# Performance work log

Measured on AMD Instinct MI355X. Metric: run time of the kernel, lower is better.

The kernel has to match this reference:

```python
import jax, jax.numpy as jnp
import numpy as np

B, S, E, H = 32, 2048, 512, 512


def setup_inputs() -> dict:
    key = jax.random.key(0)
    ks = jax.random.split(key, 6)
    scale = 1.0 / np.sqrt(H)  # PyTorch LSTM init range
    x = jax.random.normal(ks[0], (B, S, E), dtype=jnp.float32)
    lengths = jax.random.randint(ks[1], (B,), 1, S + 1, dtype=jnp.int32)
    W_ih = jax.random.uniform(ks[2], (4 * H, E), jnp.float32, -scale, scale)
    W_hh = jax.random.uniform(ks[3], (4 * H, H), jnp.float32, -scale, scale)
    b_ih = jax.random.uniform(ks[4], (4 * H,), jnp.float32, -scale, scale)
    b_hh = jax.random.uniform(ks[5], (4 * H,), jnp.float32, -scale, scale)
    return {"x": x, "lengths": lengths, "W_ih": W_ih, "W_hh": W_hh,
            "b_ih": b_ih, "b_hh": b_hh}


def _lstm_scan(x, W_ih, W_hh, b_ih, b_hh):
    # x: [B, S, E]. Precompute input projections for all timesteps (one big GEMM).
    x_proj = jnp.einsum('bse,ge->bsg', x, W_ih) + (b_ih + b_hh)  # [B, S, 4H]
    x_proj_t = jnp.swapaxes(x_proj, 0, 1)  # [S, B, 4H]

    def step(carry, xp_t):
        h, c = carry
        gates = xp_t + h @ W_hh.T  # [B, 4H]
        i, f, g, o = jnp.split(gates, 4, axis=-1)  # PyTorch gate order i,f,g,o
        i = jax.nn.sigmoid(i)
        f = jax.nn.sigmoid(f)
        g = jnp.tanh(g)
        o = jax.nn.sigmoid(o)
        c = f * c + i * g
        h = o * jnp.tanh(c)
        return (h, c), h

    h0 = jnp.zeros((B, H), dtype=x.dtype)
    c0 = jnp.zeros((B, H), dtype=x.dtype)
    (_, _), hs = jax.lax.scan(step, (h0, c0), x_proj_t)  # hs: [S, B, H]
    return hs


def reference(x, lengths, W_ih, W_hh, b_ih, b_hh):
    hs = _lstm_scan(x, W_ih, W_hh, b_ih, b_hh)  # [S, B, H]
    # zero-mask outputs at positions >= length (matches __maskLSTMOutput)
    mask = (jnp.arange(S)[:, None] < lengths[None, :]).astype(hs.dtype)  # [S, B]
    out = (hs * mask[:, :, None]).transpose(1, 0, 2)[:, :, None, :]  # [B, S, 1, H]
    # hidden state captured at t = length-1 per sequence (matches __updateHiddenOutput)
    hidden = hs[lengths - 1, jnp.arange(B)][None, :, :]  # [1, B, H]
    return (out, lengths, hidden)
```

## Files before the change

### kernel.cpp

```cpp
#include <hip/hip_runtime.h>


typedef __attribute__((ext_vector_type(8))) __bf16 bf16x8;
typedef __attribute__((ext_vector_type(8))) short short8;
typedef __attribute__((ext_vector_type(4))) float floatx4;
typedef __attribute__((ext_vector_type(2))) unsigned uint32x2;

#define XP_OFF   0ull
#define XP_BYTES (2048ull * 32ull * 2048ull * 2ull)
#define HPK_OFF  (XP_OFF + XP_BYTES)
#define HPK_BYTES (2ull * 16384ull * 8ull)
#define BIAS_OFF (HPK_OFF + HPK_BYTES)
#define WS_NEED  (BIAS_OFF + 8192ull)

#define LEN_OFF_F    33554432
#define HIDDEN_OFF_F 33554464

__device__ inline float sigm(float x) { return 1.f / (1.f + __expf(-x)); }
__device__ inline float tanh_(float x) {
  float e = __expf(-2.f * fabsf(x));
  float r = (1.f - e) / (1.f + e);
  return x >= 0.f ? r : -r;
}

__device__ inline void cvt_hilo8(const float* v, bf16x8& hi, bf16x8& lo) {
#pragma unroll
  for (int i = 0; i < 8; ++i) {
    __bf16 h = (__bf16)v[i];
    hi[i] = h;
    lo[i] = (__bf16)(v[i] - (float)h);
  }
}

__device__ inline float bf16f(unsigned short u) {
  union { unsigned u; float f; } c; c.u = ((unsigned)u) << 16; return c.f;
}

__global__ __launch_bounds__(256) void prep_kernel(
    const float* __restrict__ bih, const float* __restrict__ bhh,
    const int* __restrict__ len, float* __restrict__ biasp,
    unsigned long long* __restrict__ hpk, float* __restrict__ outf) {
  const int tid = threadIdx.x;
  for (int i = tid; i < 2048; i += 256) {
    int rowg = (i & 3) * 512 + (i >> 4) * 4 + ((i >> 2) & 3);
    biasp[i] = bih[rowg] + bhh[rowg];
  }
  for (int i = tid; i < 32768; i += 256) hpk[i] = 0ull;
  if (tid < 32) outf[LEN_OFF_F + tid] = (float)len[tid];
}

__global__ __launch_bounds__(256) void xproj_gemm(
    const float* __restrict__ x, const float* __restrict__ Wih,
    const float* __restrict__ biasp, __bf16* __restrict__ xp) {
  __shared__ short Ash[64 * 40], Asl[64 * 40], Bsh[64 * 40], Bsl[64 * 40];
  const int tid = threadIdx.x;
  const int w = tid >> 6, lane = tid & 63, ln = lane & 15, kq = lane >> 4;
  const int ntile = blockIdx.x & 31, mtile = blockIdx.x >> 5;
  const int srow = tid >> 2, sseg = tid & 3;

  const size_t a_base = (size_t)(mtile * 64 + srow) * 512 + sseg * 8;
  const int np_s = ntile * 64 + srow;
  const int rowg = (np_s & 3) * 512 + (np_s >> 4) * 4 + ((np_s >> 2) & 3);
  const size_t b_base = (size_t)rowg * 512 + sseg * 8;

  floatx4 acc[4] = {{0,0,0,0},{0,0,0,0},{0,0,0,0},{0,0,0,0}};

  for (int k0 = 0; k0 < 512; k0 += 32) {
    floatx4 a0 = *(const floatx4*)(x + a_base + k0);
    floatx4 a1 = *(const floatx4*)(x + a_base + k0 + 4);
    floatx4 b0 = *(const floatx4*)(Wih + b_base + k0);
    floatx4 b1 = *(const floatx4*)(Wih + b_base + k0 + 4);
    __syncthreads();
    {
      float va[8] = {a0[0],a0[1],a0[2],a0[3],a1[0],a1[1],a1[2],a1[3]};
      bf16x8 hi, lo; cvt_hilo8(va, hi, lo);
      *(short8*)&Ash[srow * 40 + sseg * 8] = __builtin_bit_cast(short8, hi);
      *(short8*)&Asl[srow * 40 + sseg * 8] = __builtin_bit_cast(short8, lo);
      float vb[8] = {b0[0],b0[1],b0[2],b0[3],b1[0],b1[1],b1[2],b1[3]};
      cvt_hilo8(vb, hi, lo);
      *(short8*)&Bsh[srow * 40 + sseg * 8] = __builtin_bit_cast(short8, hi);
      *(short8*)&Bsl[srow * 40 + sseg * 8] = __builtin_bit_cast(short8, lo);
    }
    __syncthreads();
    bf16x8 ah = __builtin_bit_cast(bf16x8, *(const short8*)&Ash[(16 * w + ln) * 40 + kq * 8]);
    bf16x8 al = __builtin_bit_cast(bf16x8, *(const short8*)&Asl[(16 * w + ln) * 40 + kq * 8]);
#pragma unroll
    for (int nt = 0; nt < 4; ++nt) {
      bf16x8 bh = __builtin_bit_cast(bf16x8, *(const short8*)&Bsh[(nt * 16 + ln) * 40 + kq * 8]);
      bf16x8 bl = __builtin_bit_cast(bf16x8, *(const short8*)&Bsl[(nt * 16 + ln) * 40 + kq * 8]);
      acc[nt] = __builtin_amdgcn_mfma_f32_16x16x32_bf16(ah, bh, acc[nt], 0, 0, 0);
      acc[nt] = __builtin_amdgcn_mfma_f32_16x16x32_bf16(al, bh, acc[nt], 0, 0, 0);
      acc[nt] = __builtin_amdgcn_mfma_f32_16x16x32_bf16(ah, bl, acc[nt], 0, 0, 0);
    }
  }
#pragma unroll
  for (int nt = 0; nt < 4; ++nt) {
    const int npg = ntile * 64 + nt * 16 + ln;
    const float bs = biasp[npg];
#pragma unroll
    for (int r = 0; r < 4; ++r) {
      const int m = mtile * 64 + w * 16 + kq * 4 + r;
      const int s = m & 2047, b = m >> 11;
      xp[(size_t)(s * 32 + b) * 2048 + npg] = (__bf16)(acc[nt][r] + bs);
    }
  }
}

__global__ __launch_bounds__(256, 1) void lstm_rec(
    const float* __restrict__ Whh, const int* __restrict__ lengths,
    const __bf16* __restrict__ xp, float* __restrict__ out,
    float* __restrict__ hid, unsigned long long* __restrict__ hpk) {
  __shared__ short Hh[16 * 512];
  __shared__ short Hl[16 * 512];
  __shared__ float Part[4 * 1088];

  const int tid = threadIdx.x;
  const int w = tid >> 6, lane = tid & 63, ln = lane & 15, kq = lane >> 4;
  const int bh = blockIdx.x >> 5;
  const int ug = blockIdx.x & 31;
  const int b0 = bh * 16;

  bf16x8 whi[4][4], wlo[4][4];
#pragma unroll
  for (int nt = 0; nt < 4; ++nt) {
    const int rowg = (ln & 3) * 512 + (ug * 4 + nt) * 4 + (ln >> 2);
#pragma unroll
    for (int kc = 0; kc < 4; ++kc) {
      const int h0 = w * 64 + kc * 16 + kq * 4;
      floatx4 f0 = *(const floatx4*)(Whh + (size_t)rowg * 512 + h0);
      floatx4 f1 = *(const floatx4*)(Whh + (size_t)rowg * 512 + h0 + 256);
      float v[8] = {f0[0],f1[0],f0[1],f1[1],f0[2],f1[2],f0[3],f1[3]};
      cvt_hilo8(v, whi[nt][kc], wlo[nt][kc]);
    }
  }

  const int m_e = tid >> 4, ue = tid & 15;
  const int b_e = b0 + m_e, u_e = ug * 16 + ue;
  const int lenb = lengths[b_e];
  float cst = 0.f, hcap = 0.f;

  const __bf16* xpb = xp + (size_t)b_e * 2048 + ug * 64 + (ue >> 2) * 16 + (ue & 3) * 4;
  uint32x2 xpcur = *(const uint32x2*)xpb;
  uint32x2 xpnext;

  unsigned long long* pub = hpk + b_e * 512 + u_e;
  const unsigned long long* pollb = hpk + b0 * 512 + tid;

  for (int t = 0; t < 2048; ++t) {
    {
      const int tn = (t + 1 < 2048) ? t + 1 : 2047;
      xpnext = *(const uint32x2*)(xpb + (size_t)tn * 65536);
    }
    const unsigned long long* src = pollb + (t & 1) * 16384;
    unsigned long long e[32];
    bool ok = false;
    for (;;) {
      if (!ok) {
#pragma unroll
        for (int k = 0; k < 16; ++k) {
          e[2 * k] = __hip_atomic_load(src + k * 512, __ATOMIC_RELAXED,
                                       __HIP_MEMORY_SCOPE_AGENT);
          e[2 * k + 1] = __hip_atomic_load(src + k * 512 + 256, __ATOMIC_RELAXED,
                                           __HIP_MEMORY_SCOPE_AGENT);
        }
        ok = true;
#pragma unroll
        for (int k = 0; k < 32; ++k)
          ok &= ((unsigned)(e[k] >> 32) == (unsigned)t);
      }
      if (__ballot(!ok) == 0ull) break;
      __builtin_amdgcn_s_sleep(1);
    }
    {
      const int g = tid >> 2;
#pragma unroll
      for (int k = 0; k < 16; ++k) {
        const unsigned d0 = (unsigned)e[2 * k], d1 = (unsigned)e[2 * k + 1];
        const int d = k * 512 + ((g ^ (k & 7)) * 8) + (tid & 3) * 2;
        *(unsigned*)&Hh[d] = (d0 >> 16) | (d1 & 0xffff0000u);
        *(unsigned*)&Hl[d] = (d0 & 0xffffu) | (d1 << 16);
      }
    }
    __syncthreads();
    floatx4 acc[4] = {{0,0,0,0},{0,0,0,0},{0,0,0,0},{0,0,0,0}};
#pragma unroll
    for (int kc = 0; kc < 4; ++kc) {
      const int g = w * 16 + kc * 4 + kq;
      const int d = ln * 512 + ((g ^ (ln & 7)) * 8);
      bf16x8 ah = __builtin_bit_cast(bf16x8, *(const short8*)&Hh[d]);
      bf16x8 al = __builtin_bit_cast(bf16x8, *(const short8*)&Hl[d]);
#pragma unroll
      for (int nt = 0; nt < 4; ++nt) {
        acc[nt] = __builtin_amdgcn_mfma_f32_16x16x32_bf16(ah, whi[nt][kc], acc[nt], 0, 0, 0);
        acc[nt] = __builtin_amdgcn_mfma_f32_16x16x32_bf16(al, whi[nt][kc], acc[nt], 0, 0, 0);
        acc[nt] = __builtin_amdgcn_mfma_f32_16x16x32_bf16(ah, wlo[nt][kc], acc[nt], 0, 0, 0);
      }
    }
#pragma unroll
    for (int nt = 0; nt < 4; ++nt)
#pragma unroll
      for (int r4 = 0; r4 < 4; ++r4)
        Part[w * 1088 + nt * 272 + (kq * 4 + r4) * 16 + ln] = acc[nt][r4];
    __syncthreads();
    {
      const int pb = (ue >> 2) * 272 + m_e * 16 + (ue & 3) * 4;
      floatx4 p0 = *(const floatx4*)&Part[pb];
      floatx4 p1 = *(const floatx4*)&Part[1088 + pb];
      floatx4 p2 = *(const floatx4*)&Part[2176 + pb];
      floatx4 p3 = *(const floatx4*)&Part[3264 + pb];
      const float xg0 = bf16f((unsigned short)(xpcur[0] & 0xffffu));
      const float xg1 = bf16f((unsigned short)(xpcur[0] >> 16));
      const float xg2 = bf16f((unsigned short)(xpcur[1] & 0xffffu));
      const float xg3 = bf16f((unsigned short)(xpcur[1] >> 16));
      const float pi = xg0 + p0[0] + p1[0] + p2[0] + p3[0];
      const float pf = xg1 + p0[1] + p1[1] + p2[1] + p3[1];
      const float pg = xg2 + p0[2] + p1[2] + p2[2] + p3[2];
      const float po = xg3 + p0[3] + p1[3] + p2[3] + p3[3];
      const float gi_ = sigm(pi), gf = sigm(pf), gg = tanh_(pg), go = sigm(po);
      cst = gf * cst + gi_ * gg;
      const float hv = go * tanh_(cst);
      const __bf16 hb = (__bf16)hv;
      const __bf16 lb = (__bf16)(hv - (float)hb);
      const unsigned pk =
          ((unsigned)__builtin_bit_cast(unsigned short, hb) << 16) |
          (unsigned)__builtin_bit_cast(unsigned short, lb);
      __hip_atomic_store(pub + ((t + 1) & 1) * 16384,
                         ((unsigned long long)(unsigned)(t + 1) << 32) |
                             (unsigned long long)pk,
                         __ATOMIC_RELAXED, __HIP_MEMORY_SCOPE_AGENT);
      out[((size_t)b_e * 2048 + t) * 512 + u_e] = (t < lenb) ? hv : 0.f;
      if (t == lenb - 1) hcap = hv;
    }
    xpcur = xpnext;
  }
  hid[b_e * 512 + u_e] = hcap;
}

extern "C" void kernel_launch(void* const* d_in, const int* in_sizes, int n_in,
                              void* d_out, int out_size, void* d_ws, size_t ws_size,
                              hipStream_t stream) {
  const float* x = (const float*)d_in[0];
  const int* lengths = (const int*)d_in[1];
  const float* Wih = (const float*)d_in[2];
  const float* Whh = (const float*)d_in[3];
  const float* bih = (const float*)d_in[4];
  const float* bhh = (const float*)d_in[5];
  float* outf = (float*)d_out;
  char* ws = (char*)d_ws;
  if (ws_size < WS_NEED) return;

  float* biasp = (float*)(ws + BIAS_OFF);
  __bf16* xp = (__bf16*)(ws + XP_OFF);
  unsigned long long* hpk = (unsigned long long*)(ws + HPK_OFF);

  prep_kernel<<<1, 256, 0, stream>>>(bih, bhh, lengths, biasp, hpk, outf);
  xproj_gemm<<<32768, 256, 0, stream>>>(x, Wih, biasp, xp);
  lstm_rec<<<64, 256, 0, stream>>>(Whh, lengths, xp, outf,
                                   outf + HIDDEN_OFF_F, hpk);
}
```

Before: 8.097 ms.

## Add transposed fast h-exchange buffer with vector nontemporal polling and slow fallback

Measured after the change: 18.88 ms. 2.33x slower.

```diff
diff --git a/kernel.cpp b/kernel.cpp
--- a/kernel.cpp
+++ b/kernel.cpp
@@ -5,13 +5,16 @@
 typedef __attribute__((ext_vector_type(8))) short short8;
 typedef __attribute__((ext_vector_type(4))) float floatx4;
 typedef __attribute__((ext_vector_type(2))) unsigned uint32x2;
-
-#define XP_OFF   0ull
-#define XP_BYTES (2048ull * 32ull * 2048ull * 2ull)
-#define HPK_OFF  (XP_OFF + XP_BYTES)
-#define HPK_BYTES (2ull * 16384ull * 8ull)
-#define BIAS_OFF (HPK_OFF + HPK_BYTES)
-#define WS_NEED  (BIAS_OFF + 8192ull)
+typedef __attribute__((ext_vector_type(4))) unsigned uint32x4;
+
+#define XP_OFF     0ull
+#define XP_BYTES   (2048ull * 32ull * 2048ull * 2ull)
+#define FAST_OFF   (XP_OFF + XP_BYTES)
+#define FAST_BYTES (2ull * 512ull * 32ull * 8ull)
+#define SLOW_OFF   (FAST_OFF + FAST_BYTES)
+#define SLOW_BYTES (2ull * 32ull * 512ull * 8ull)
+#define BIAS_OFF   (SLOW_OFF + SLOW_BYTES)
+#define WS_NEED    (BIAS_OFF + 8192ull)
 
 #define LEN_OFF_F    33554432
 #define HIDDEN_OFF_F 33554464
@@ -39,14 +42,16 @@
 __global__ __launch_bounds__(256) void prep_kernel(
     const float* __restrict__ bih, const float* __restrict__ bhh,
     const int* __restrict__ len, float* __restrict__ biasp,
-    unsigned long long* __restrict__ hpk, float* __restrict__ outf) {
-  const int tid = threadIdx.x;
-  for (int i = tid; i < 2048; i += 256) {
+    unsigned long long* __restrict__ hreg,
+    float* __restrict__ outf) {
+  const int gtid = blockIdx.x * 256 + threadIdx.x;
+  if (gtid < 2048) {
+    int i = gtid;
     int rowg = (i & 3) * 512 + (i >> 4) * 4 + ((i >> 2) & 3);
     biasp[i] = bih[rowg] + bhh[rowg];
   }
-  for (int i = tid; i < 32768; i += 256) hpk[i] = 0ull;
-  if (tid < 32) outf[LEN_OFF_F + tid] = (float)len[tid];
+  for (int i = gtid; i < 65536; i += 16384) hreg[i] = 0ull;
+  if (gtid < 32) outf[LEN_OFF_F + gtid] = (float)len[gtid];
 }
 
 __global__ __launch_bounds__(256) void xproj_gemm(
@@ -109,15 +114,22 @@
 __global__ __launch_bounds__(256, 1) void lstm_rec(
     const float* __restrict__ Whh, const int* __restrict__ lengths,
     const __bf16* __restrict__ xp, float* __restrict__ out,
-    float* __restrict__ hid, unsigned long long* __restrict__ hpk) {
+    float* __restrict__ hid, unsigned long long* __restrict__ fastR,
+    unsigned long long* __restrict__ slowR) {
   __shared__ short Hh[16 * 512];
   __shared__ short Hl[16 * 512];
   __shared__ float Part[4 * 1088];
+  __shared__ volatile char ldspad[36864];
+
+  const int blk = blockIdx.x;
+  const int bh = blk & 7;
+  const int ug = blk >> 3;
+  if (bh >= 2 || ug >= 32) return;
 
   const int tid = threadIdx.x;
+  if (tid == 0) ldspad[0] = 1;
+
   const int w = tid >> 6, lane = tid & 63, ln = lane & 15, kq = lane >> 4;
-  const int bh = blockIdx.x >> 5;
-  const int ug = blockIdx.x & 31;
   const int b0 = bh * 16;
 
   bf16x8 whi[4][4], wlo[4][4];
@@ -143,39 +155,77 @@
   uint32x2 xpcur = *(const uint32x2*)xpb;
   uint32x2 xpnext;
 
-  unsigned long long* pub = hpk + b_e * 512 + u_e;
-  const unsigned long long* pollb = hpk + b0 * 512 + tid;
+  const char* Fb = (const char*)fastR;
+  char* fpub_base = (char*)fastR + ((size_t)u_e * 32 + b_e) * 8;
+  unsigned long long* spub_base = slowR + (size_t)b_e * 512 + u_e;
+
+  int fastmode = 1;
 
   for (int t = 0; t < 2048; ++t) {
     {
       const int tn = (t + 1 < 2048) ? t + 1 : 2047;
       xpnext = *(const uint32x2*)(xpb + (size_t)tn * 65536);
     }
-    const unsigned long long* src = pollb + (t & 1) * 16384;
-    unsigned long long e[32];
-    bool ok = false;
-    for (;;) {
-      if (!ok) {
+    unsigned pk0[16], pk1[16];
+    uint32x4 q[16];
+    if (fastmode) {
+      const uint32x4* fb0 = (const uint32x4*)(Fb + (size_t)(t & 1) * 131072 +
+                                              (size_t)tid * 256 + (size_t)b0 * 8);
+      const uint32x4* fb1 = (const uint32x4*)((const char*)fb0 + 65536);
+      int spins = 0;
+      for (;;) {
+        bool ok = true;
+#pragma unroll
+        for (int j = 0; j < 8; ++j) {
+          q[j] = __builtin_nontemporal_load(fb0 + j);
+          q[8 + j] = __builtin_nontemporal_load(fb1 + j);
+        }
+#pragma unroll
+        for (int j = 0; j < 16; ++j)
+          ok = ok && (q[j][1] == (unsigned)t) && (q[j][3] == (unsigned)t);
+        if (ok) break;
+        if (++spins > 256) { fastmode = 0; break; }
+        __builtin_amdgcn_s_sleep(2);
+        asm volatile("" ::: "memory");
+      }
+    }
+    if (fastmode) {
+#pragma unroll
+      for (int j = 0; j < 8; ++j) {
+        pk0[2 * j] = q[j][0];
+        pk0[2 * j + 1] = q[j][2];
+        pk1[2 * j] = q[8 + j][0];
+        pk1[2 * j + 1] = q[8 + j][2];
+      }
+    } else {
+      const unsigned long long* sb = slowR + (size_t)(t & 1) * 16384 + b0 * 512;
+      unsigned long long e[32];
+      for (;;) {
+        bool ok = true;
 #pragma unroll
         for (int k = 0; k < 16; ++k) {
-          e[2 * k] = __hip_atomic_load(src + k * 512, __ATOMIC_RELAXED,
-                                       __HIP_MEMORY_SCOPE_AGENT);
-          e[2 * k + 1] = __hip_atomic_load(src + k * 512 + 256, __ATOMIC_RELAXED,
-                                           __HIP_MEMORY_SCOPE_AGENT);
+          e[2 * k] = __hip_atomic_load(sb + (size_t)k * 512 + tid,
+                                       __ATOMIC_RELAXED, __HIP_MEMORY_SCOPE_AGENT);
+          e[2 * k + 1] = __hip_atomic_load(sb + (size_t)k * 512 + tid + 256,
+                                           __ATOMIC_RELAXED, __HIP_MEMORY_SCOPE_AGENT);
         }
-        ok = true;
 #pragma unroll
         for (int k = 0; k < 32; ++k)
-          ok &= ((unsigned)(e[k] >> 32) == (unsigned)t);
-      }
-      if (__ballot(!ok) == 0ull) break;
-      __builtin_amdgcn_s_sleep(1);
+          ok = ok && ((unsigned)(e[k] >> 32) == (unsigned)t);
+        if (ok) break;
+        __builtin_amdgcn_s_sleep(4);
+      }
+#pragma unroll
+      for (int k = 0; k < 16; ++k) {
+        pk0[k] = (unsigned)e[2 * k];
+        pk1[k] = (unsigned)e[2 * k + 1];
+      }
     }
     {
       const int g = tid >> 2;
 #pragma unroll
       for (int k = 0; k < 16; ++k) {
-        const unsigned d0 = (unsigned)e[2 * k], d1 = (unsigned)e[2 * k + 1];
+        const unsigned d0 = pk0[k], d1 = pk1[k];
         const int d = k * 512 + ((g ^ (k & 7)) * 8) + (tid & 3) * 2;
         *(unsigned*)&Hh[d] = (d0 >> 16) | (d1 & 0xffff0000u);
         *(unsigned*)&Hl[d] = (d0 & 0xffffu) | (d1 << 16);
@@ -224,9 +274,11 @@
       const unsigned pk =
           ((unsigned)__builtin_bit_cast(unsigned short, hb) << 16) |
           (unsigned)__builtin_bit_cast(unsigned short, lb);
-      __hip_atomic_store(pub + ((t + 1) & 1) * 16384,
-                         ((unsigned long long)(unsigned)(t + 1) << 32) |
-                             (unsigned long long)pk,
+      const unsigned long long ent =
+          ((unsigned long long)(unsigned)(t + 1) << 32) | (unsigned long long)pk;
+      *(volatile unsigned long long*)(fpub_base +
+                                      (size_t)((t + 1) & 1) * 131072) = ent;
+      __hip_atomic_store(spub_base + (size_t)((t + 1) & 1) * 16384, ent,
                          __ATOMIC_RELAXED, __HIP_MEMORY_SCOPE_AGENT);
       out[((size_t)b_e * 2048 + t) * 512 + u_e] = (t < lenb) ? hv : 0.f;
       if (t == lenb - 1) hcap = hv;
@@ -251,10 +303,11 @@
 
   float* biasp = (float*)(ws + BIAS_OFF);
   __bf16* xp = (__bf16*)(ws + XP_OFF);
-  unsigned long long* hpk = (unsigned long long*)(ws + HPK_OFF);
-
-  prep_kernel<<<1, 256, 0, stream>>>(bih, bhh, lengths, biasp, hpk, outf);
+  unsigned long long* fastR = (unsigned long long*)(ws + FAST_OFF);
+  unsigned long long* slowR = (unsigned long long*)(ws + SLOW_OFF);
+
+  prep_kernel<<<64, 256, 0, stream>>>(bih, bhh, lengths, biasp, fastR, outf);
   xproj_gemm<<<32768, 256, 0, stream>>>(x, Wih, biasp, xp);
-  lstm_rec<<<64, 256, 0, stream>>>(Whh, lengths, xp, outf,
-                                   outf + HIDDEN_OFF_F, hpk);
-}
+  lstm_rec<<<256, 256, 0, stream>>>(Whh, lengths, xp, outf,
+                                    outf + HIDDEN_OFF_F, fastR, slowR);
+}
```
